# Kernel tuning notes

Hardware: AMD Instinct MI355X
Metric: run time of the kernel (lower is better)

Reference implementation:

```python
import jax, jax.numpy as jnp
import numpy as np

M = 256       # number of chart centers
D = 512       # feature dim
B = 131072    # batch of encoder features
R = 32.0      # chart radius (~sqrt(2*D) for whitened random data)
TAU = 0.01    # center EMA rate
EPS = 1e-6


def setup_inputs() -> dict:
    key = jax.random.key(0)
    k0, k1, k2, k3 = jax.random.split(key, 4)
    z = jax.random.normal(k0, (B, D), dtype=jnp.float32)
    centers = jax.random.normal(k1, (M, D), dtype=jnp.float32)
    stats_mean = 0.1 * jax.random.normal(k2, (D,), dtype=jnp.float32)
    stats_var = jax.random.uniform(k3, (D,), dtype=jnp.float32, minval=0.5, maxval=1.5)
    return {"z": z, "centers": centers, "stats_mean": stats_mean, "stats_var": stats_var}


def _whiten(z, mean, var):
    return (z - mean) / jnp.sqrt(var + EPS)


def _cdist(z_w, centers):
    # ||a-c||^2 = ||a||^2 + ||c||^2 - 2 a.c   (avoids [B,M,D] intermediate)
    zn = jnp.sum(z_w * z_w, axis=1)            # [B]
    cn = jnp.sum(centers * centers, axis=1)     # [M]
    d2 = zn[:, None] + cn[None, :] - 2.0 * (z_w @ centers.T)  # [B, M]
    return jnp.sqrt(jnp.maximum(d2, 0.0))


def reference(z, centers, stats_mean, stats_var):
    # memberships(): whiten + cdist + argmin + radius masks
    z_w = _whiten(z, stats_mean, stats_var)     # [B, D]
    dists = _cdist(z_w, centers)                # [B, M]
    hard_idx = jnp.argmin(dists, axis=1)        # [B]
    masks = dists <= R                          # [B, M] bool (masks[:, i] == torch masks[i])

    # soft_update_centers(): scatter-mean of z_w per nearest cluster, EMA update
    counts = jax.ops.segment_sum(jnp.ones((z_w.shape[0],), z_w.dtype), hard_idx, num_segments=M)  # [M]
    sums = jax.ops.segment_sum(z_w, hard_idx, num_segments=M)                                     # [M, D]
    mean_i = sums / jnp.maximum(counts, 1.0)[:, None]
    has_members = (counts > 0)[:, None]
    new_centers = jnp.where(has_members, (1.0 - TAU) * centers + TAU * mean_i, centers)

    return dists, hard_idx, masks, new_centers
```

## Files before the change

### kernel.cpp

```cpp
#include <hip/hip_runtime.h>
#include <math.h>

#define M_CENTERS 256
#define D_DIM     512
#define B_BATCH   131072
#define RADIUS    32.0f
#define TAU_F     0.01f
#define EPS_F     1e-6f

#define DMARGIN 1.0e-3f
#define REF_BLOCKS 256
#define UCHUNKS 16
#define NCHUNK 32
#define SC_ROWS 1024

typedef __attribute__((ext_vector_type(8))) short bf16x8;
typedef __attribute__((ext_vector_type(16))) float f32x16;

__device__ __forceinline__ unsigned short bf16h(float x) {
    unsigned int u = __float_as_uint(x);
    return (unsigned short)((u + 0x7fffu + ((u >> 16) & 1u)) >> 16);
}
__device__ __forceinline__ float bf16tof(unsigned short h) {
    return __uint_as_float(((unsigned int)h) << 16);
}
__device__ __forceinline__ unsigned cvt_pk_bf16(float a, float b) {
    unsigned r;
    asm("v_cvt_pk_bf16_f32 %0, %1, %2" : "=v"(r) : "v"(a), "v"(b));
    return r;
}

__global__ void prep_ss_kernel(const float* __restrict__ mean, const float* __restrict__ var,
                               float* __restrict__ scale, float* __restrict__ shift) {
    int d = blockIdx.x * 256 + threadIdx.x;
    if (d < D_DIM) {
        float s = 1.0f / sqrtf(var[d] + EPS_F);
        scale[d] = s;
        shift[d] = -mean[d] * s;
    }
}

__global__ void prep_cb_kernel(const float* __restrict__ centers, unsigned char* __restrict__ img,
                               float* __restrict__ cn) {
    int c = blockIdx.x;
    int l = threadIdx.x;
    int kc = l >> 1, kg = l & 1;
    const float* cp = centers + (size_t)c * D_DIM + kc * 16 + kg * 8;
    float4 a = *reinterpret_cast<const float4*>(cp);
    float4 b = *reinterpret_cast<const float4*>(cp + 4);
    float x0 = a.x, x1 = a.y, x2 = a.z, x3 = a.w, x4 = b.x, x5 = b.y, x6 = b.z, x7 = b.w;
    float s = x0*x0 + x1*x1 + x2*x2 + x3*x3 + x4*x4 + x5*x5 + x6*x6 + x7*x7;
    #pragma unroll
    for (int off = 32; off >= 1; off >>= 1) s += __shfl_xor(s, off, 64);
    if (l == 0) cn[c] = s;

    unsigned short h0 = bf16h(x0), h1 = bf16h(x1), h2 = bf16h(x2), h3 = bf16h(x3);
    unsigned short h4 = bf16h(x4), h5 = bf16h(x5), h6 = bf16h(x6), h7 = bf16h(x7);
    unsigned short g0 = bf16h(x0 - bf16tof(h0)), g1 = bf16h(x1 - bf16tof(h1));
    unsigned short g2 = bf16h(x2 - bf16tof(h2)), g3 = bf16h(x3 - bf16tof(h3));
    unsigned short g4 = bf16h(x4 - bf16tof(h4)), g5 = bf16h(x5 - bf16tof(h5));
    unsigned short g6 = bf16h(x6 - bf16tof(h6)), g7 = bf16h(x7 - bf16tof(h7));
    size_t base = (size_t)kc * 16384 + (size_t)c * 32 + (size_t)kg * 16;
    *reinterpret_cast<uint4*>(img + base) =
        make_uint4((unsigned)h0 | ((unsigned)h1 << 16), (unsigned)h2 | ((unsigned)h3 << 16),
                   (unsigned)h4 | ((unsigned)h5 << 16), (unsigned)h6 | ((unsigned)h7 << 16));
    *reinterpret_cast<uint4*>(img + 8192 + base) =
        make_uint4((unsigned)g0 | ((unsigned)g1 << 16), (unsigned)g2 | ((unsigned)g3 << 16),
                   (unsigned)g4 | ((unsigned)g5 << 16), (unsigned)g6 | ((unsigned)g7 << 16));
}

__global__ __launch_bounds__(256, 4)
void dist_mfma_kernel(const float* __restrict__ z,
                      const unsigned char* __restrict__ cb_img,
                      const float* __restrict__ scale, const float* __restrict__ shift,
                      const float* __restrict__ cn,
                      float* __restrict__ out_dists, float* __restrict__ out_idxf,
                      float* __restrict__ out_masks, int* __restrict__ ws_idx,
                      int* __restrict__ amb_count, int* __restrict__ amb_rows) {
    __shared__ union {
        struct { unsigned char A[2][4096]; unsigned char B[2][16384]; } p;
        float bounce[2][16][256];
        struct { float znrow[64]; float rminS[64][2]; int ridxS[64][2];
                 int rcntS[64][2]; float fminS[64]; } e;
    } sm;

    const int tid = threadIdx.x;
    const int wv = tid >> 6, lane = tid & 63;
    const int rt = wv >> 1, ch = wv & 1;
    const int l31 = lane & 31, kg = lane >> 5;
    const int b0 = blockIdx.x * 64;

    const int arow = tid >> 2, akq = tid & 3;
    const float* zrow = z + (size_t)(b0 + arow) * D_DIM;

    f32x16 acc[4];
    #pragma unroll
    for (int n = 0; n < 4; ++n)
        #pragma unroll
        for (int r = 0; r < 16; ++r) acc[n][r] = 0.0f;
    float zsq = 0.0f;
    float4 zv, scv, shv;

    auto stage_load = [&](int kc, int cb) {
        const unsigned char* bsrc = cb_img + (size_t)kc * 16384 + (size_t)wv * 4096;
        unsigned char* bdst = &sm.p.B[cb][wv * 4096];
        #pragma unroll
        for (int r = 0; r < 4; ++r) {
            __builtin_amdgcn_global_load_lds(
                (const __attribute__((address_space(1))) unsigned int*)(bsrc + r * 1024 + (lane << 4)),
                (__attribute__((address_space(3))) unsigned int*)(bdst + r * 1024),
                16, 0, 0);
        }
        const int kf = kc * 16 + akq * 4;
        zv  = *reinterpret_cast<const float4*>(zrow + kf);
        scv = *reinterpret_cast<const float4*>(scale + kf);
        shv = *reinterpret_cast<const float4*>(shift + kf);
    };
    auto stage_write = [&](int cb) {
        float w0 = fmaf(zv.x, scv.x, shv.x);
        float w1 = fmaf(zv.y, scv.y, shv.y);
        float w2 = fmaf(zv.z, scv.z, shv.z);
        float w3 = fmaf(zv.w, scv.w, shv.w);
        zsq = fmaf(w0, w0, fmaf(w1, w1, fmaf(w2, w2, fmaf(w3, w3, zsq))));
        unsigned hv0 = cvt_pk_bf16(w0, w1);
        unsigned hv1 = cvt_pk_bf16(w2, w3);
        float r0 = __uint_as_float(hv0 << 16);
        float r1 = __uint_as_float(hv0 & 0xffff0000u);
        float r2 = __uint_as_float(hv1 << 16);
        float r3 = __uint_as_float(hv1 & 0xffff0000u);
        unsigned lv0 = cvt_pk_bf16(w0 - r0, w1 - r1);
        unsigned lv1 = cvt_pk_bf16(w2 - r2, w3 - r3);
        *reinterpret_cast<uint2*>(&sm.p.A[cb][arow * 32 + akq * 8]) = make_uint2(hv0, hv1);
        *reinterpret_cast<uint2*>(&sm.p.A[cb][2048 + arow * 32 + akq * 8]) = make_uint2(lv0, lv1);
    };

    stage_load(0, 0);
    stage_write(0);
    __syncthreads();

    int cc = 0;
    for (int kc = 0; kc < NCHUNK; ++kc) {
        const bool pf = (kc + 1 < NCHUNK);
        if (pf) stage_load(kc + 1, cc ^ 1);
        const unsigned char* Ab = &sm.p.A[cc][0];
        const int aoff = (rt * 32 + l31) * 32 + kg * 16;
        bf16x8 a_hi = *reinterpret_cast<const bf16x8*>(Ab + aoff);
        bf16x8 a_lo = *reinterpret_cast<const bf16x8*>(Ab + 2048 + aoff);
        const unsigned char* Bb = &sm.p.B[cc][0];
        #pragma unroll
        for (int n = 0; n < 4; ++n) {
            const int boff = (ch * 128 + n * 32 + l31) * 32 + kg * 16;
            bf16x8 b_hi = *reinterpret_cast<const bf16x8*>(Bb + boff);
            bf16x8 b_lo = *reinterpret_cast<const bf16x8*>(Bb + 8192 + boff);
            acc[n] = __builtin_amdgcn_mfma_f32_32x32x16_bf16(a_hi, b_hi, acc[n], 0, 0, 0);
            acc[n] = __builtin_amdgcn_mfma_f32_32x32x16_bf16(a_hi, b_lo, acc[n], 0, 0, 0);
            acc[n] = __builtin_amdgcn_mfma_f32_32x32x16_bf16(a_lo, b_hi, acc[n], 0, 0, 0);
        }
        if (pf) stage_write(cc ^ 1);
        __syncthreads();
        cc ^= 1;
    }

    zsq += __shfl_xor(zsq, 1, 64);
    zsq += __shfl_xor(zsq, 2, 64);
    if (akq == 0) sm.e.znrow[arow] = zsq;
    __syncthreads();

    float znv[16];
    #pragma unroll
    for (int r = 0; r < 16; ++r) znv[r] = sm.e.znrow[rt * 32 + 4 * kg + (r & 3) + 8 * (r >> 2)];
    float cnv[4];
    #pragma unroll
    for (int n = 0; n < 4; ++n) cnv[n] = cn[ch * 128 + n * 32 + l31];

    #pragma unroll
    for (int n = 0; n < 4; ++n)
        #pragma unroll
        for (int r = 0; r < 16; ++r) {
            float d2 = znv[r] + cnv[n] - 2.0f * acc[n][r];
            acc[n][r] = sqrtf(fmaxf(d2, 0.0f));
        }

    #pragma unroll
    for (int r = 0; r < 16; ++r) {
        float bd = 3.4e38f; int bi = 0;
        #pragma unroll
        for (int n = 0; n < 4; ++n) {
            float d = acc[n][r];
            int col = ch * 128 + n * 32 + l31;
            if (d < bd) { bd = d; bi = col; }
        }
        #pragma unroll
        for (int off = 1; off <= 16; off <<= 1) {
            float od = __shfl_xor(bd, off, 64);
            int   oi = __shfl_xor(bi, off, 64);
            if (od < bd || (od == bd && oi < bi)) { bd = od; bi = oi; }
        }
        if (l31 == 0) {
            int R = rt * 32 + 4 * kg + (r & 3) + 8 * (r >> 2);
            sm.e.rminS[R][ch] = bd; sm.e.ridxS[R][ch] = bi;
        }
    }
    __syncthreads();
    if (tid < 64) {
        float d0 = sm.e.rminS[tid][0], d1 = sm.e.rminS[tid][1];
        int i0 = sm.e.ridxS[tid][0], i1 = sm.e.ridxS[tid][1];
        float fd = d0; int fi = i0;
        if (d1 < d0 || (d1 == d0 && i1 < i0)) { fd = d1; fi = i1; }
        sm.e.fminS[tid] = fd;
        out_idxf[b0 + tid] = (float)fi;
        ws_idx[b0 + tid] = fi;
    }
    __syncthreads();
    #pragma unroll
    for (int r = 0; r < 16; ++r) {
        int R = rt * 32 + 4 * kg + (r & 3) + 8 * (r >> 2);
        float thr = sm.e.fminS[R] + DMARGIN;
        int cnt = 0;
        #pragma unroll
        for (int n = 0; n < 4; ++n) cnt += (acc[n][r] <= thr) ? 1 : 0;
        #pragma unroll
        for (int off = 1; off <= 16; off <<= 1) cnt += __shfl_xor(cnt, off, 64);
        if (l31 == 0) sm.e.rcntS[R][ch] = cnt;
    }
    __syncthreads();
    if (tid < 64) {
        if (sm.e.rcntS[tid][0] + sm.e.rcntS[tid][1] > 1) {
            int p = atomicAdd(amb_count, 1);
            if (p < B_BATCH) amb_rows[p] = b0 + tid;
        }
    }

    #pragma unroll
    for (int hp = 0; hp < 2; ++hp) {
        __syncthreads();
        #pragma unroll
        for (int rr = 0; rr < 8; ++rr) {
            const int r = hp * 8 + rr;
            const int Rl = 4 * kg + (r & 3) + 8 * (r >> 2) - hp * 16;
            #pragma unroll
            for (int n = 0; n < 4; ++n)
                sm.bounce[rt][Rl][ch * 128 + n * 32 + l31] = acc[n][r];
        }
        __syncthreads();
        #pragma unroll
        for (int i = 0; i < 8; ++i) {
            const int Rl = ch * 8 + i;
            float4 dq = *reinterpret_cast<const float4*>(&sm.bounce[rt][Rl][lane * 4]);
            const int grow = b0 + rt * 32 + hp * 16 + Rl;
            size_t ob = (size_t)grow * M_CENTERS + lane * 4;
            *reinterpret_cast<float4*>(out_dists + ob) = dq;
            float4 mq = make_float4(dq.x <= RADIUS ? 1.0f : 0.0f, dq.y <= RADIUS ? 1.0f : 0.0f,
                                    dq.z <= RADIUS ? 1.0f : 0.0f, dq.w <= RADIUS ? 1.0f : 0.0f);
            *reinterpret_cast<float4*>(out_masks + ob) = mq;
        }
    }
}

__global__ __launch_bounds__(64)
void refine_kernel(const float* __restrict__ z, const float* __restrict__ centers,
                   const float* __restrict__ smean, const float* __restrict__ svar,
                   const float* __restrict__ dists,
                   const int* __restrict__ amb_count, const int* __restrict__ amb_rows,
                   float* __restrict__ out_idxf, int* __restrict__ ws_idx) {
    const int lane = threadIdx.x;
    int n = *amb_count;
    if (n > B_BATCH) n = B_BATCH;
    for (int e = blockIdx.x; e < n; e += REF_BLOCKS) {
        const int row = amb_rows[e];
        float4 dq = *reinterpret_cast<const float4*>(dists + (size_t)row * M_CENTERS + lane * 4);
        float dl[4] = { dq.x, dq.y, dq.z, dq.w };
        float dmin = fminf(fminf(dl[0], dl[1]), fminf(dl[2], dl[3]));
        #pragma unroll
        for (int off = 32; off >= 1; off >>= 1) dmin = fminf(dmin, __shfl_xor(dmin, off, 64));

        float zwf[8];
        double zn = 0.0;
        {
            float4 za = *reinterpret_cast<const float4*>(z + (size_t)row * D_DIM + lane * 8);
            float4 zb = *reinterpret_cast<const float4*>(z + (size_t)row * D_DIM + lane * 8 + 4);
            float zr[8] = { za.x, za.y, za.z, za.w, zb.x, zb.y, zb.z, zb.w };
            #pragma unroll
            for (int k = 0; k < 8; ++k) {
                int d = lane * 8 + k;
                float w = (zr[k] - smean[d]) / sqrtf(svar[d] + EPS_F);
                zwf[k] = w;
                zn += (double)w * (double)w;
            }
        }
        #pragma unroll
        for (int off = 32; off >= 1; off >>= 1) zn += __shfl_xor(zn, off, 64);
        const float zn32 = (float)zn;

        float bestd = 3.4e38f;
        int bestj = M_CENTERS;
        #pragma unroll
        for (int q = 0; q < 4; ++q) {
            unsigned long long mask = __ballot(dl[q] <= dmin + DMARGIN);
            while (mask) {
                int b = __ffsll(mask) - 1;
                mask &= mask - 1;
                int j = b * 4 + q;
                float4 ca = *reinterpret_cast<const float4*>(centers + (size_t)j * D_DIM + lane * 8);
                float4 cb = *reinterpret_cast<const float4*>(centers + (size_t)j * D_DIM + lane * 8 + 4);
                float cr[8] = { ca.x, ca.y, ca.z, ca.w, cb.x, cb.y, cb.z, cb.w };
                double dot = 0.0, cnl = 0.0;
                #pragma unroll
                for (int k = 0; k < 8; ++k) {
                    double c = (double)cr[k];
                    dot += (double)zwf[k] * c;
                    cnl += c * c;
                }
                #pragma unroll
                for (int off = 32; off >= 1; off >>= 1) {
                    dot += __shfl_xor(dot, off, 64);
                    cnl += __shfl_xor(cnl, off, 64);
                }
                float cn32  = (float)cnl;
                float dot32 = (float)dot;
                float t1  = zn32 + cn32;
                float d2f = t1 - 2.0f * dot32;
                d2f = fmaxf(d2f, 0.0f);
                float df = sqrtf(d2f);
                if (df < bestd || (df == bestd && j < bestj)) { bestd = df; bestj = j; }
            }
        }
        if (lane == 0) {
            out_idxf[row] = (float)bestj;
            ws_idx[row]   = bestj;
        }
    }
}

__global__ void hist_kernel(const int* __restrict__ idx, int* __restrict__ counts) {
    __shared__ int h[M_CENTERS];
    h[threadIdx.x] = 0;
    __syncthreads();
    int base = blockIdx.x * 512;
    atomicAdd(&h[idx[base + threadIdx.x]], 1);
    atomicAdd(&h[idx[base + 256 + threadIdx.x]], 1);
    __syncthreads();
    int c = h[threadIdx.x];
    if (c) atomicAdd(&counts[threadIdx.x], c);
}

__global__ void scan_kernel(const int* __restrict__ counts, int* __restrict__ offsets,
                            int* __restrict__ cursor) {
    __shared__ int s[M_CENTERS];
    int t = threadIdx.x;
    int c = counts[t];
    s[t] = c;
    __syncthreads();
    for (int off = 1; off < M_CENTERS; off <<= 1) {
        int v = (t >= off) ? s[t - off] : 0;
        __syncthreads();
        s[t] += v;
        __syncthreads();
    }
    int excl = s[t] - c;
    offsets[t] = excl;
    cursor[t]  = excl;
    if (t == M_CENTERS - 1) offsets[M_CENTERS] = s[t];
}

__global__ __launch_bounds__(256)
void scatter2_kernel(const int* __restrict__ idx, int* __restrict__ cursor,
                     int* __restrict__ order) {
    __shared__ int lh[M_CENTERS];
    __shared__ int lb[M_CENTERS];
    const int t = threadIdx.x;
    lh[t] = 0;
    __syncthreads();
    const int base = blockIdx.x * SC_ROWS;
    int m[4], pl[4];
    #pragma unroll
    for (int k = 0; k < 4; ++k) {
        m[k] = idx[base + k * 256 + t];
        pl[k] = atomicAdd(&lh[m[k]], 1);
    }
    __syncthreads();
    int c = lh[t];
    if (c > 0) lb[t] = atomicAdd(&cursor[t], c);
    __syncthreads();
    #pragma unroll
    for (int k = 0; k < 4; ++k)
        order[lb[m[k]] + pl[k]] = base + k * 256 + t;
}

__global__ __launch_bounds__(128)
void update_partial_kernel(const float* __restrict__ z,
                           const float* __restrict__ scale, const float* __restrict__ shift,
                           const int* __restrict__ offsets, const int* __restrict__ order,
                           float* __restrict__ partial) {
    const int m = blockIdx.x / UCHUNKS;
    const int c = blockIdx.x % UCHUNKS;
    const int t = threadIdx.x;
    const int d0 = t * 4;
    const int start = offsets[m], end = offsets[m + 1];
    const int len = end - start;
    const int cs = (len + UCHUNKS - 1) / UCHUNKS;
    const int s0 = start + c * cs;
    int s1 = s0 + cs; if (s1 > end) s1 = end;

    const float4 sc = *reinterpret_cast<const float4*>(scale + d0);
    const float4 sh = *reinterpret_cast<const float4*>(shift + d0);
    float a0 = 0.0f, a1 = 0.0f, a2 = 0.0f, a3 = 0.0f;
    int i = s0;
    for (; i + 4 <= s1; i += 4) {
        int b0 = order[i], b1 = order[i + 1], b2 = order[i + 2], b3 = order[i + 3];
        float4 v0 = *reinterpret_cast<const float4*>(z + (size_t)b0 * D_DIM + d0);
        float4 v1 = *reinterpret_cast<const float4*>(z + (size_t)b1 * D_DIM + d0);
        float4 v2 = *reinterpret_cast<const float4*>(z + (size_t)b2 * D_DIM + d0);
        float4 v3 = *reinterpret_cast<const float4*>(z + (size_t)b3 * D_DIM + d0);
        a0 += fmaf(v0.x, sc.x, sh.x); a1 += fmaf(v0.y, sc.y, sh.y);
        a2 += fmaf(v0.z, sc.z, sh.z); a3 += fmaf(v0.w, sc.w, sh.w);
        a0 += fmaf(v1.x, sc.x, sh.x); a1 += fmaf(v1.y, sc.y, sh.y);
        a2 += fmaf(v1.z, sc.z, sh.z); a3 += fmaf(v1.w, sc.w, sh.w);
        a0 += fmaf(v2.x, sc.x, sh.x); a1 += fmaf(v2.y, sc.y, sh.y);
        a2 += fmaf(v2.z, sc.z, sh.z); a3 += fmaf(v2.w, sc.w, sh.w);
        a0 += fmaf(v3.x, sc.x, sh.x); a1 += fmaf(v3.y, sc.y, sh.y);
        a2 += fmaf(v3.z, sc.z, sh.z); a3 += fmaf(v3.w, sc.w, sh.w);
    }
    for (; i < s1; ++i) {
        int b = order[i];
        float4 v = *reinterpret_cast<const float4*>(z + (size_t)b * D_DIM + d0);
        a0 += fmaf(v.x, sc.x, sh.x); a1 += fmaf(v.y, sc.y, sh.y);
        a2 += fmaf(v.z, sc.z, sh.z); a3 += fmaf(v.w, sc.w, sh.w);
    }
    *reinterpret_cast<float4*>(partial + ((size_t)blockIdx.x) * D_DIM + d0) =
        make_float4(a0, a1, a2, a3);
}

__global__ __launch_bounds__(128)
void update_reduce_kernel(const float* __restrict__ centers,
                          const int* __restrict__ offsets,
                          const float* __restrict__ partial,
                          float* __restrict__ out_nc) {
    const int m = blockIdx.x;
    const int t = threadIdx.x;
    const int d0 = t * 4;
    const int cnt = offsets[m + 1] - offsets[m];
    float a0 = 0.0f, a1 = 0.0f, a2 = 0.0f, a3 = 0.0f;
    #pragma unroll
    for (int c = 0; c < UCHUNKS; ++c) {
        float4 v = *reinterpret_cast<const float4*>(partial + ((size_t)(m * UCHUNKS + c)) * D_DIM + d0);
        a0 += v.x; a1 += v.y; a2 += v.z; a3 += v.w;
    }
    float4 cv = *reinterpret_cast<const float4*>(centers + (size_t)m * D_DIM + d0);
    float4 r = cv;
    if (cnt > 0) {
        float inv = 1.0f / (float)cnt;
        r.x = (1.0f - TAU_F) * cv.x + TAU_F * (a0 * inv);
        r.y = (1.0f - TAU_F) * cv.y + TAU_F * (a1 * inv);
        r.z = (1.0f - TAU_F) * cv.z + TAU_F * (a2 * inv);
        r.w = (1.0f - TAU_F) * cv.w + TAU_F * (a3 * inv);
    }
    *reinterpret_cast<float4*>(out_nc + (size_t)m * D_DIM + d0) = r;
}

extern "C" void kernel_launch(void* const* d_in, const int* in_sizes, int n_in,
                              void* d_out, int out_size, void* d_ws, size_t ws_size,
                              hipStream_t stream) {
    const float* z       = (const float*)d_in[0];
    const float* centers = (const float*)d_in[1];
    const float* smean   = (const float*)d_in[2];
    const float* svar    = (const float*)d_in[3];

    float* out = (float*)d_out;
    float* out_dists = out;
    float* out_idxf  = out + (size_t)B_BATCH * M_CENTERS;
    float* out_masks = out_idxf + B_BATCH;
    float* out_nc    = out_masks + (size_t)B_BATCH * M_CENTERS;

    char* wsp = (char*)d_ws;
    float* scale   = (float*)wsp; wsp += D_DIM * sizeof(float);
    float* shift   = (float*)wsp; wsp += D_DIM * sizeof(float);
    float* cn      = (float*)wsp; wsp += M_CENTERS * sizeof(float);
    int* ws_idx    = (int*)wsp;   wsp += (size_t)B_BATCH * sizeof(int);
    int* counts    = (int*)wsp;   wsp += M_CENTERS * sizeof(int);
    int* offsets   = (int*)wsp;   wsp += (M_CENTERS + 4) * sizeof(int);
    int* cursor    = (int*)wsp;   wsp += M_CENTERS * sizeof(int);
    int* amb_count = (int*)wsp;   wsp += 4 * sizeof(int);
    int* order     = (int*)wsp;   wsp += (size_t)B_BATCH * sizeof(int);
    int* amb_rows  = (int*)wsp;   wsp += (size_t)B_BATCH * sizeof(int);
    float* partial = (float*)wsp; wsp += (size_t)M_CENTERS * UCHUNKS * D_DIM * sizeof(float);
    unsigned char* cb_img = (unsigned char*)wsp; wsp += (size_t)NCHUNK * 16384;

    prep_ss_kernel<<<2, 256, 0, stream>>>(smean, svar, scale, shift);
    prep_cb_kernel<<<M_CENTERS, 64, 0, stream>>>(centers, cb_img, cn);
    hipMemsetAsync(amb_count, 0, sizeof(int), stream);
    hipMemsetAsync(counts, 0, M_CENTERS * sizeof(int), stream);
    dist_mfma_kernel<<<B_BATCH / 64, 256, 0, stream>>>(z, cb_img, scale, shift, cn,
                                                       out_dists, out_idxf, out_masks, ws_idx,
                                                       amb_count, amb_rows);
    refine_kernel<<<REF_BLOCKS, 64, 0, stream>>>(z, centers, smean, svar, out_dists,
                                                 amb_count, amb_rows, out_idxf, ws_idx);
    hist_kernel<<<B_BATCH / 512, 256, 0, stream>>>(ws_idx, counts);
    scan_kernel<<<1, 256, 0, stream>>>(counts, offsets, cursor);
    scatter2_kernel<<<B_BATCH / SC_ROWS, 256, 0, stream>>>(ws_idx, cursor, order);
    update_partial_kernel<<<M_CENTERS * UCHUNKS, 128, 0, stream>>>(z, scale, shift,
                                                                   offsets, order, partial);
    update_reduce_kernel<<<M_CENTERS, 128, 0, stream>>>(centers, offsets, partial, out_nc);
}
```

Baseline: 316.5 us.

## Drop split-bf16 GEMM to single bf16, fuse histogram into distance kernel

Replaces the three-pass hi/lo bf16 split product with a single bf16 MFMA pass per k-slice. The K-chunk doubles to 32 and the smem layouts for A and B are changed to match. The ambiguity margin is widened and refine blocks are increased so exact fp32 refinement can still correct argmin errors. The cluster histogram moves into the distance kernel via an LDS histogram, and the refine kernel patches counts atomically, so the separate hist kernel and one memset go away. The risk is lower distance precision in the output dists and many more rows sent to refinement.

```diff
diff --git a/kernel.cpp b/kernel.cpp
--- a/kernel.cpp
+++ b/kernel.cpp
@@ -8,10 +8,10 @@
 #define TAU_F     0.01f
 #define EPS_F     1e-6f
 
-#define DMARGIN 1.0e-3f
-#define REF_BLOCKS 256
+#define DMARGIN 2.0e-2f
+#define REF_BLOCKS 1024
 #define UCHUNKS 16
-#define NCHUNK 32
+#define NCHUNK 16
 #define SC_ROWS 1024
 
 typedef __attribute__((ext_vector_type(8))) short bf16x8;
@@ -20,9 +20,6 @@
 __device__ __forceinline__ unsigned short bf16h(float x) {
     unsigned int u = __float_as_uint(x);
     return (unsigned short)((u + 0x7fffu + ((u >> 16) & 1u)) >> 16);
-}
-__device__ __forceinline__ float bf16tof(unsigned short h) {
-    return __uint_as_float(((unsigned int)h) << 16);
 }
 __device__ __forceinline__ unsigned cvt_pk_bf16(float a, float b) {
     unsigned r;
@@ -44,29 +41,21 @@
                                float* __restrict__ cn) {
     int c = blockIdx.x;
     int l = threadIdx.x;
-    int kc = l >> 1, kg = l & 1;
-    const float* cp = centers + (size_t)c * D_DIM + kc * 16 + kg * 8;
+    int kc = l >> 2, kq = l & 3;
+    const float* cp = centers + (size_t)c * D_DIM + kc * 32 + kq * 8;
     float4 a = *reinterpret_cast<const float4*>(cp);
     float4 b = *reinterpret_cast<const float4*>(cp + 4);
-    float x0 = a.x, x1 = a.y, x2 = a.z, x3 = a.w, x4 = b.x, x5 = b.y, x6 = b.z, x7 = b.w;
-    float s = x0*x0 + x1*x1 + x2*x2 + x3*x3 + x4*x4 + x5*x5 + x6*x6 + x7*x7;
+    float s = a.x*a.x + a.y*a.y + a.z*a.z + a.w*a.w + b.x*b.x + b.y*b.y + b.z*b.z + b.w*b.w;
     #pragma unroll
     for (int off = 32; off >= 1; off >>= 1) s += __shfl_xor(s, off, 64);
     if (l == 0) cn[c] = s;
 
-    unsigned short h0 = bf16h(x0), h1 = bf16h(x1), h2 = bf16h(x2), h3 = bf16h(x3);
-    unsigned short h4 = bf16h(x4), h5 = bf16h(x5), h6 = bf16h(x6), h7 = bf16h(x7);
-    unsigned short g0 = bf16h(x0 - bf16tof(h0)), g1 = bf16h(x1 - bf16tof(h1));
-    unsigned short g2 = bf16h(x2 - bf16tof(h2)), g3 = bf16h(x3 - bf16tof(h3));
-    unsigned short g4 = bf16h(x4 - bf16tof(h4)), g5 = bf16h(x5 - bf16tof(h5));
-    unsigned short g6 = bf16h(x6 - bf16tof(h6)), g7 = bf16h(x7 - bf16tof(h7));
-    size_t base = (size_t)kc * 16384 + (size_t)c * 32 + (size_t)kg * 16;
-    *reinterpret_cast<uint4*>(img + base) =
-        make_uint4((unsigned)h0 | ((unsigned)h1 << 16), (unsigned)h2 | ((unsigned)h3 << 16),
-                   (unsigned)h4 | ((unsigned)h5 << 16), (unsigned)h6 | ((unsigned)h7 << 16));
-    *reinterpret_cast<uint4*>(img + 8192 + base) =
-        make_uint4((unsigned)g0 | ((unsigned)g1 << 16), (unsigned)g2 | ((unsigned)g3 << 16),
-                   (unsigned)g4 | ((unsigned)g5 << 16), (unsigned)g6 | ((unsigned)g7 << 16));
+    unsigned h0 = cvt_pk_bf16(a.x, a.y);
+    unsigned h1 = cvt_pk_bf16(a.z, a.w);
+    unsigned h2 = cvt_pk_bf16(b.x, b.y);
+    unsigned h3 = cvt_pk_bf16(b.z, b.w);
+    *reinterpret_cast<uint4*>(img + (size_t)kc * 16384 + (size_t)kq * 4096 + (size_t)c * 16) =
+        make_uint4(h0, h1, h2, h3);
 }
 
 __global__ __launch_bounds__(256, 4)
@@ -76,12 +65,13 @@
                       const float* __restrict__ cn,
                       float* __restrict__ out_dists, float* __restrict__ out_idxf,
                       float* __restrict__ out_masks, int* __restrict__ ws_idx,
+                      int* __restrict__ counts,
                       int* __restrict__ amb_count, int* __restrict__ amb_rows) {
     __shared__ union {
         struct { unsigned char A[2][4096]; unsigned char B[2][16384]; } p;
         float bounce[2][16][256];
         struct { float znrow[64]; float rminS[64][2]; int ridxS[64][2];
-                 int rcntS[64][2]; float fminS[64]; } e;
+                 int rcntS[64][2]; float fminS[64]; int lhist[M_CENTERS]; } e;
     } sm;
 
     const int tid = threadIdx.x;
@@ -99,7 +89,7 @@
         #pragma unroll
         for (int r = 0; r < 16; ++r) acc[n][r] = 0.0f;
     float zsq = 0.0f;
-    float4 zv, scv, shv;
+    float4 zv, zv2, scv, scv2, shv, shv2;
 
     auto stage_load = [&](int kc, int cb) {
         const unsigned char* bsrc = cb_img + (size_t)kc * 16384 + (size_t)wv * 4096;
@@ -111,27 +101,28 @@
                 (__attribute__((address_space(3))) unsigned int*)(bdst + r * 1024),
                 16, 0, 0);
         }
-        const int kf = kc * 16 + akq * 4;
-        zv  = *reinterpret_cast<const float4*>(zrow + kf);
-        scv = *reinterpret_cast<const float4*>(scale + kf);
-        shv = *reinterpret_cast<const float4*>(shift + kf);
+        const int kf = kc * 32 + akq * 8;
+        zv   = *reinterpret_cast<const float4*>(zrow + kf);
+        zv2  = *reinterpret_cast<const float4*>(zrow + kf + 4);
+        scv  = *reinterpret_cast<const float4*>(scale + kf);
+        scv2 = *reinterpret_cast<const float4*>(scale + kf + 4);
+        shv  = *reinterpret_cast<const float4*>(shift + kf);
+        shv2 = *reinterpret_cast<const float4*>(shift + kf + 4);
     };
     auto stage_write = [&](int cb) {
-        float w0 = fmaf(zv.x, scv.x, shv.x);
-        float w1 = fmaf(zv.y, scv.y, shv.y);
-        float w2 = fmaf(zv.z, scv.z, shv.z);
-        float w3 = fmaf(zv.w, scv.w, shv.w);
+        float w0 = fmaf(zv.x,  scv.x,  shv.x);
+        float w1 = fmaf(zv.y,  scv.y,  shv.y);
+        float w2 = fmaf(zv.z,  scv.z,  shv.z);
+        float w3 = fmaf(zv.w,  scv.w,  shv.w);
+        float w4 = fmaf(zv2.x, scv2.x, shv2.x);
+        float w5 = fmaf(zv2.y, scv2.y, shv2.y);
+        float w6 = fmaf(zv2.z, scv2.z, shv2.z);
+        float w7 = fmaf(zv2.w, scv2.w, shv2.w);
         zsq = fmaf(w0, w0, fmaf(w1, w1, fmaf(w2, w2, fmaf(w3, w3, zsq))));
-        unsigned hv0 = cvt_pk_bf16(w0, w1);
-        unsigned hv1 = cvt_pk_bf16(w2, w3);
-        float r0 = __uint_as_float(hv0 << 16);
-        float r1 = __uint_as_float(hv0 & 0xffff0000u);
-        float r2 = __uint_as_float(hv1 << 16);
-        float r3 = __uint_as_float(hv1 & 0xffff0000u);
-        unsigned lv0 = cvt_pk_bf16(w0 - r0, w1 - r1);
-        unsigned lv1 = cvt_pk_bf16(w2 - r2, w3 - r3);
-        *reinterpret_cast<uint2*>(&sm.p.A[cb][arow * 32 + akq * 8]) = make_uint2(hv0, hv1);
-        *reinterpret_cast<uint2*>(&sm.p.A[cb][2048 + arow * 32 + akq * 8]) = make_uint2(lv0, lv1);
+        zsq = fmaf(w4, w4, fmaf(w5, w5, fmaf(w6, w6, fmaf(w7, w7, zsq))));
+        uint4 hv = make_uint4(cvt_pk_bf16(w0, w1), cvt_pk_bf16(w2, w3),
+                              cvt_pk_bf16(w4, w5), cvt_pk_bf16(w6, w7));
+        *reinterpret_cast<uint4*>(&sm.p.A[cb][akq * 1024 + arow * 16]) = hv;
     };
 
     stage_load(0, 0);
@@ -143,18 +134,17 @@
         const bool pf = (kc + 1 < NCHUNK);
         if (pf) stage_load(kc + 1, cc ^ 1);
         const unsigned char* Ab = &sm.p.A[cc][0];
-        const int aoff = (rt * 32 + l31) * 32 + kg * 16;
-        bf16x8 a_hi = *reinterpret_cast<const bf16x8*>(Ab + aoff);
-        bf16x8 a_lo = *reinterpret_cast<const bf16x8*>(Ab + 2048 + aoff);
         const unsigned char* Bb = &sm.p.B[cc][0];
+        const int arow16 = (rt * 32 + l31) * 16;
+        bf16x8 a0 = *reinterpret_cast<const bf16x8*>(Ab + (0 * 2 + kg) * 1024 + arow16);
+        bf16x8 a1 = *reinterpret_cast<const bf16x8*>(Ab + (1 * 2 + kg) * 1024 + arow16);
         #pragma unroll
         for (int n = 0; n < 4; ++n) {
-            const int boff = (ch * 128 + n * 32 + l31) * 32 + kg * 16;
-            bf16x8 b_hi = *reinterpret_cast<const bf16x8*>(Bb + boff);
-            bf16x8 b_lo = *reinterpret_cast<const bf16x8*>(Bb + 8192 + boff);
-            acc[n] = __builtin_amdgcn_mfma_f32_32x32x16_bf16(a_hi, b_hi, acc[n], 0, 0, 0);
-            acc[n] = __builtin_amdgcn_mfma_f32_32x32x16_bf16(a_hi, b_lo, acc[n], 0, 0, 0);
-            acc[n] = __builtin_amdgcn_mfma_f32_32x32x16_bf16(a_lo, b_hi, acc[n], 0, 0, 0);
+            const int bcol16 = (ch * 128 + n * 32 + l31) * 16;
+            bf16x8 b0 = *reinterpret_cast<const bf16x8*>(Bb + (0 * 2 + kg) * 4096 + bcol16);
+            bf16x8 b1 = *reinterpret_cast<const bf16x8*>(Bb + (1 * 2 + kg) * 4096 + bcol16);
+            acc[n] = __builtin_amdgcn_mfma_f32_32x32x16_bf16(a0, b0, acc[n], 0, 0, 0);
+            acc[n] = __builtin_amdgcn_mfma_f32_32x32x16_bf16(a1, b1, acc[n], 0, 0, 0);
         }
         if (pf) stage_write(cc ^ 1);
         __syncthreads();
@@ -164,6 +154,7 @@
     zsq += __shfl_xor(zsq, 1, 64);
     zsq += __shfl_xor(zsq, 2, 64);
     if (akq == 0) sm.e.znrow[arow] = zsq;
+    sm.e.lhist[tid] = 0;
     __syncthreads();
 
     float znv[16];
@@ -210,6 +201,7 @@
         sm.e.fminS[tid] = fd;
         out_idxf[b0 + tid] = (float)fi;
         ws_idx[b0 + tid] = fi;
+        atomicAdd(&sm.e.lhist[fi], 1);
     }
     __syncthreads();
     #pragma unroll
@@ -230,6 +222,7 @@
             if (p < B_BATCH) amb_rows[p] = b0 + tid;
         }
     }
+    if (sm.e.lhist[tid] > 0) atomicAdd(&counts[tid], sm.e.lhist[tid]);
 
     #pragma unroll
     for (int hp = 0; hp < 2; ++hp) {
@@ -262,7 +255,8 @@
                    const float* __restrict__ smean, const float* __restrict__ svar,
                    const float* __restrict__ dists,
                    const int* __restrict__ amb_count, const int* __restrict__ amb_rows,
-                   float* __restrict__ out_idxf, int* __restrict__ ws_idx) {
+                   float* __restrict__ out_idxf, int* __restrict__ ws_idx,
+                   int* __restrict__ counts) {
     const int lane = threadIdx.x;
     int n = *amb_count;
     if (n > B_BATCH) n = B_BATCH;
@@ -326,22 +320,15 @@
             }
         }
         if (lane == 0) {
-            out_idxf[row] = (float)bestj;
-            ws_idx[row]   = bestj;
-        }
-    }
-}
-
-__global__ void hist_kernel(const int* __restrict__ idx, int* __restrict__ counts) {
-    __shared__ int h[M_CENTERS];
-    h[threadIdx.x] = 0;
-    __syncthreads();
-    int base = blockIdx.x * 512;
-    atomicAdd(&h[idx[base + threadIdx.x]], 1);
-    atomicAdd(&h[idx[base + 256 + threadIdx.x]], 1);
-    __syncthreads();
-    int c = h[threadIdx.x];
-    if (c) atomicAdd(&counts[threadIdx.x], c);
+            int old = ws_idx[row];
+            if (old != bestj) {
+                atomicSub(&counts[old], 1);
+                atomicAdd(&counts[bestj], 1);
+                out_idxf[row] = (float)bestj;
+                ws_idx[row]   = bestj;
+            }
+        }
+    }
 }
 
 __global__ void scan_kernel(const int* __restrict__ counts, int* __restrict__ offsets,
@@ -478,9 +465,9 @@
     float* cn      = (float*)wsp; wsp += M_CENTERS * sizeof(float);
     int* ws_idx    = (int*)wsp;   wsp += (size_t)B_BATCH * sizeof(int);
     int* counts    = (int*)wsp;   wsp += M_CENTERS * sizeof(int);
+    int* amb_count = (int*)wsp;   wsp += 4 * sizeof(int);
     int* offsets   = (int*)wsp;   wsp += (M_CENTERS + 4) * sizeof(int);
     int* cursor    = (int*)wsp;   wsp += M_CENTERS * sizeof(int);
-    int* amb_count = (int*)wsp;   wsp += 4 * sizeof(int);
     int* order     = (int*)wsp;   wsp += (size_t)B_BATCH * sizeof(int);
     int* amb_rows  = (int*)wsp;   wsp += (size_t)B_BATCH * sizeof(int);
     float* partial = (float*)wsp; wsp += (size_t)M_CENTERS * UCHUNKS * D_DIM * sizeof(float);
@@ -488,14 +475,12 @@
 
     prep_ss_kernel<<<2, 256, 0, stream>>>(smean, svar, scale, shift);
     prep_cb_kernel<<<M_CENTERS, 64, 0, stream>>>(centers, cb_img, cn);
-    hipMemsetAsync(amb_count, 0, sizeof(int), stream);
-    hipMemsetAsync(counts, 0, M_CENTERS * sizeof(int), stream);
+    hipMemsetAsync(counts, 0, (M_CENTERS + 4) * sizeof(int), stream);
     dist_mfma_kernel<<<B_BATCH / 64, 256, 0, stream>>>(z, cb_img, scale, shift, cn,
                                                        out_dists, out_idxf, out_masks, ws_idx,
-                                                       amb_count, amb_rows);
+                                                       counts, amb_count, amb_rows);
     refine_kernel<<<REF_BLOCKS, 64, 0, stream>>>(z, centers, smean, svar, out_dists,
-                                                 amb_count, amb_rows, out_idxf, ws_idx);
-    hist_kernel<<<B_BATCH / 512, 256, 0, stream>>>(ws_idx, counts);
+                                                 amb_count, amb_rows, out_idxf, ws_idx, counts);
     scan_kernel<<<1, 256, 0, stream>>>(counts, offsets, cursor);
     scatter2_kernel<<<B_BATCH / SC_ROWS, 256, 0, stream>>>(ws_idx, cursor, order);
     update_partial_kernel<<<M_CENTERS * UCHUNKS, 128, 0, stream>>>(z, scale, shift,
```

Measured after the change: 308.7 us. -2.4%, faster.
